# Kernel optimization log

Measured on AMD Instinct MI355X. Metric: run time of the kernel, lower is better.

## Reference

```python
import jax, jax.numpy as jnp
import numpy as np

LOGIT_SCALE_MAX = float(np.log(1.0 / 0.01))  # log(100)
EPS = 1e-12  # F.normalize eps


def setup_inputs() -> dict:
    key = jax.random.key(0)
    ks = jax.random.split(key, 4)
    L, N, C, H = 1024, 8, 1024, 16
    x = jax.random.normal(ks[0], (L, N, C), dtype=jnp.float32)
    w_in = jax.random.normal(ks[1], (3 * C, C), dtype=jnp.float32) * 0.02
    b_in = jnp.zeros((3 * C,), dtype=jnp.float32)
    logit_scale = jnp.full((H, 1, 1), float(np.log(10.0)), dtype=jnp.float32)
    head_scale = jnp.ones((H, 1, 1), dtype=jnp.float32)
    w_out = jax.random.normal(ks[2], (C, C), dtype=jnp.float32) * 0.02
    b_out = jnp.zeros((C,), dtype=jnp.float32)
    return {"x": x, "w_in": w_in, "b_in": b_in, "logit_scale": logit_scale,
            "head_scale": head_scale, "w_out": w_out, "b_out": b_out}


def _l2norm(t):
    # matches F.normalize(t, dim=-1): t / max(||t||, eps)
    n = jnp.sqrt(jnp.sum(t * t, axis=-1, keepdims=True))
    return t / jnp.maximum(n, EPS)


def reference(x, w_in, b_in, logit_scale, head_scale, w_out, b_out):
    L, N, C = x.shape
    H = logit_scale.shape[0]
    D = C // H
    qkv = x @ w_in.T + b_in                      # (L, N, 3C)
    q, k, v = jnp.split(qkv, 3, axis=-1)         # each (L, N, C)

    def to_heads(t):                             # (L, N, C) -> (N*H, L, D)
        return t.reshape(L, N * H, D).transpose(1, 0, 2)

    q, k, v = to_heads(q), to_heads(k), to_heads(v)
    # cosine-similarity logits with clamped learned per-head scale
    attn = jnp.einsum('bld,bmd->blm', _l2norm(q), _l2norm(k))  # (N*H, L, L)
    ls = jnp.exp(jnp.minimum(logit_scale, LOGIT_SCALE_MAX))    # (H,1,1)
    attn = (attn.reshape(N, H, L, L) * ls).reshape(N * H, L, L)
    attn = jax.nn.softmax(attn, axis=-1)
    out = jnp.einsum('blm,bmd->bld', attn, v)    # (N*H, L, D)
    # per-head scaling (intended math of the head_scale branch)
    out = (out.reshape(N, H, L, D) * head_scale).reshape(N * H, L, D)
    out = out.transpose(1, 0, 2).reshape(L, N, C)
    out = out @ w_out.T + b_out
    return out, attn
```

## Files before the change

kernel.cpp:

```cpp
#include <hip/hip_runtime.h>
#include <hip/hip_fp16.h>
#include <cstdint>

typedef _Float16 f16;
typedef _Float16 f16x8 __attribute__((ext_vector_type(8)));
typedef float f32x4 __attribute__((ext_vector_type(4)));

#define MFMA16(a, b, c) __builtin_amdgcn_mfma_f32_16x16x32_f16(a, b, c, 0, 0, 0)

constexpr int Lq = 1024, Nb = 8, Cc = 1024, Hh = 16, Dd = 64;
constexpr int Mrows = Lq * Nb;
constexpr float LOG100 = 4.6051701859880913680f;
constexpr float LOG2E = 1.4426950408889634f;

typedef const __attribute__((address_space(1))) unsigned int* gu32p;
typedef __attribute__((address_space(3))) unsigned int* lu32p;
__device__ __forceinline__ void gl_lds16(const void* g, void* l) {
  __builtin_amdgcn_global_load_lds((gu32p)g, (lu32p)l, 16, 0, 0);
}

__global__ __launch_bounds__(256) void k_cvt(const float* __restrict__ in,
                                             f16* __restrict__ out, int n8) {
  int i = blockIdx.x * blockDim.x + threadIdx.x;
  if (i >= n8) return;
  const float4* p = (const float4*)in + (size_t)i * 2;
  float4 a = p[0], b = p[1];
  f16x8 o = {(f16)a.x, (f16)a.y, (f16)a.z, (f16)a.w,
             (f16)b.x, (f16)b.y, (f16)b.z, (f16)b.w};
  *((f16x8*)out + i) = o;
}

template <typename OutT>
__global__ __launch_bounds__(256) void k_gemm(const f16* __restrict__ A,
                                              const f16* __restrict__ B,
                                              const float* __restrict__ bias,
                                              OutT* __restrict__ Co,
                                              int Np, int Kd) {
  __shared__ f16 Ash[128 * 64];
  __shared__ f16 Bsh[128 * 64];
  const int tid = threadIdx.x, lane = tid & 63, wid = tid >> 6;
  const int m0 = blockIdx.y * 128, n0 = blockIdx.x * 128;
  const int wy = wid >> 1, wx = wid & 1;
  const int rq = lane & 15, kq = lane >> 4;
  f32x4 acc[4][4] = {};
  const int nkt = Kd >> 6;
  for (int kt = 0; kt < nkt; ++kt) {
    __syncthreads();
    for (int iss = 0; iss < 4; ++iss) {
      int cbase = (iss * 4 + wid) * 64;
      int c = cbase + lane;
      int row = ((c >> 7) << 4) + (c & 15);
      int col = kt * 64 + ((c >> 6) & 1) * 32 + ((c >> 4) & 3) * 8;
      gl_lds16(A + (size_t)(m0 + row) * Kd + col, (char*)Ash + cbase * 16);
      gl_lds16(B + (size_t)(n0 + row) * Kd + col, (char*)Bsh + cbase * 16);
    }
    __syncthreads();
    for (int ks = 0; ks < 2; ++ks) {
      f16x8 af[4], bf[4];
      for (int t = 0; t < 4; ++t)
        af[t] = *(const f16x8*)((const char*)Ash + ((((wy * 4 + t) * 2 + ks) * 64 + lane) * 16));
      for (int u = 0; u < 4; ++u)
        bf[u] = *(const f16x8*)((const char*)Bsh + ((((wx * 4 + u) * 2 + ks) * 64 + lane) * 16));
      for (int t = 0; t < 4; ++t)
        for (int u = 0; u < 4; ++u)
          acc[t][u] = MFMA16(af[t], bf[u], acc[t][u]);
    }
  }
  for (int t = 0; t < 4; ++t) {
    int row = m0 + wy * 64 + t * 16 + 4 * kq;
    for (int u = 0; u < 4; ++u) {
      int col = n0 + wx * 64 + u * 16 + rq;
      float bv = bias[col];
      for (int rr = 0; rr < 4; ++rr) {
        float v = acc[t][u][rr] + bv;
        Co[(size_t)(row + rr) * Np + col] = (OutT)v;
      }
    }
  }
}

__global__ __launch_bounds__(256) void k_norm(const f16* __restrict__ qkv,
                                              f16* __restrict__ qhat,
                                              f16* __restrict__ khat,
                                              f16* __restrict__ vTt) {
  __shared__ f16 vt[64][72];
  const int blk = blockIdx.x;
  const int b = blk >> 4, lc = blk & 15;
  const int h = b & 15, n = b >> 4;
  const int tid = threadIdx.x;
  const int g4 = tid >> 2, sub = tid & 3;
  const int lrow = lc * 64 + g4;
  const size_t srow = ((size_t)lrow * Nb + n) * 3072;
  for (int qk = 0; qk < 2; ++qk) {
    const f16* p = qkv + srow + qk * 1024 + h * 64 + sub * 16;
    f16x8 a = *(const f16x8*)p;
    f16x8 c2 = *(const f16x8*)(p + 8);
    float ss = 0.f;
    for (int e = 0; e < 8; ++e) { float x = (float)a[e]; ss += x * x; }
    for (int e = 0; e < 8; ++e) { float x = (float)c2[e]; ss += x * x; }
    ss += __shfl_xor(ss, 1);
    ss += __shfl_xor(ss, 2);
    float sc = 1.f / fmaxf(sqrtf(ss), 1e-12f);
    f16x8 oa, ob;
    for (int e = 0; e < 8; ++e) oa[e] = (f16)((float)a[e] * sc);
    for (int e = 0; e < 8; ++e) ob[e] = (f16)((float)c2[e] * sc);
    f16* dst = (qk ? khat : qhat) + ((size_t)b * Lq + lrow) * Dd + sub * 16;
    *(f16x8*)dst = oa;
    *(f16x8*)(dst + 8) = ob;
  }
  {
    const f16* p = qkv + srow + 2048 + h * 64 + sub * 16;
    f16x8 a = *(const f16x8*)p;
    f16x8 c2 = *(const f16x8*)(p + 8);
    for (int e = 0; e < 8; ++e) vt[g4][sub * 16 + e] = a[e];
    for (int e = 0; e < 8; ++e) vt[g4][sub * 16 + 8 + e] = c2[e];
  }
  __syncthreads();
  {
    const int d = g4;
    f16x8 oa, ob;
    for (int e = 0; e < 8; ++e) oa[e] = vt[sub * 16 + e][d];
    for (int e = 0; e < 8; ++e) ob[e] = vt[sub * 16 + 8 + e][d];
    f16* dst = vTt + ((size_t)b * Dd + d) * Lq + lc * 64 + sub * 16;
    *(f16x8*)dst = oa;
    *(f16x8*)(dst + 8) = ob;
  }
}

__global__ __launch_bounds__(256) void k_attn(const f16* __restrict__ qhat,
                                              const f16* __restrict__ khat,
                                              const f16* __restrict__ vTt,
                                              const float* __restrict__ lsc,
                                              const float* __restrict__ hsc,
                                              float* __restrict__ attn,
                                              f16* __restrict__ Ows) {
  __shared__ float plds[4][16 * 68];
  const int blk = blockIdx.x;
  const int b = blk >> 4, qc = blk & 15;
  const int h = b & 15, n = b >> 4;
  const int tid = threadIdx.x, lane = tid & 63, w = tid >> 6;
  const int rq = lane & 15, kq = lane >> 4;
  const int ib = qc * 64 + w * 16;
  const float ls = __expf(fminf(lsc[h], LOG100));
  const float hs = hsc[h];
  const float c1 = ls * LOG2E, c0 = -c1;
  const f16* qb = qhat + ((size_t)b * Lq + ib) * Dd;
  f16x8 qf0 = *(const f16x8*)(qb + (size_t)rq * Dd + kq * 8);
  f16x8 qf1 = *(const f16x8*)(qb + (size_t)rq * Dd + 32 + kq * 8);
  const f16* kb = khat + (size_t)b * Lq * Dd;
  float lsum[4] = {0.f, 0.f, 0.f, 0.f};
  for (int kt = 0; kt < 16; ++kt) {
    const int j0 = kt * 64;
    f32x4 s[4];
    for (int u = 0; u < 4; ++u) {
      const f16* kp = kb + (size_t)(j0 + u * 16 + rq) * Dd + kq * 8;
      f16x8 k0 = *(const f16x8*)kp;
      f16x8 k1 = *(const f16x8*)(kp + 32);
      f32x4 a = {0.f, 0.f, 0.f, 0.f};
      a = MFMA16(qf0, k0, a);
      a = MFMA16(qf1, k1, a);
      s[u] = a;
    }
    for (int rr = 0; rr < 4; ++rr) {
      float e0 = exp2f(fmaf(s[0][rr], c1, c0));
      float e1 = exp2f(fmaf(s[1][rr], c1, c0));
      float e2 = exp2f(fmaf(s[2][rr], c1, c0));
      float e3 = exp2f(fmaf(s[3][rr], c1, c0));
      lsum[rr] += (e0 + e1) + (e2 + e3);
    }
  }
  float invl[4];
  for (int rr = 0; rr < 4; ++rr) {
    float l = lsum[rr];
    l += __shfl_xor(l, 1);
    l += __shfl_xor(l, 2);
    l += __shfl_xor(l, 4);
    l += __shfl_xor(l, 8);
    invl[rr] = 1.f / l;
  }
  float* pw = plds[w];
  f32x4 Oa[4] = {};
  const f16* vb = vTt + (size_t)b * Dd * Lq;
  float* ab = attn + (size_t)b * Lq * Lq;
  const int srow = lane >> 2, sc4 = lane & 3;
  for (int kt = 0; kt < 16; ++kt) {
    const int j0 = kt * 64;
    f32x4 s[4];
    for (int u = 0; u < 4; ++u) {
      const f16* kp = kb + (size_t)(j0 + u * 16 + rq) * Dd + kq * 8;
      f16x8 k0 = *(const f16x8*)kp;
      f16x8 k1 = *(const f16x8*)(kp + 32);
      f32x4 a = {0.f, 0.f, 0.f, 0.f};
      a = MFMA16(qf0, k0, a);
      a = MFMA16(qf1, k1, a);
      s[u] = a;
    }
    for (int u = 0; u < 4; ++u)
      for (int rr = 0; rr < 4; ++rr) {
        float p = exp2f(fmaf(s[u][rr], c1, c0)) * invl[rr];
        pw[(4 * kq + rr) * 68 + u * 16 + rq] = p;
      }
    {
      const float* lp = pw + srow * 68;
      float* gp = ab + (size_t)(ib + srow) * Lq + j0;
      for (int st = 0; st < 4; ++st) {
        int f4 = st * 4 + sc4;
        f32x4 v = *(const f32x4*)(lp + f4 * 4);
        *(f32x4*)(gp + f4 * 4) = v;
      }
    }
    f16x8 pa[2];
    for (int ks = 0; ks < 2; ++ks) {
      const float* sp = pw + rq * 68 + ks * 32 + kq * 8;
      f16x8 t;
      for (int e = 0; e < 8; ++e) t[e] = (f16)sp[e];
      pa[ks] = t;
    }
    for (int t = 0; t < 4; ++t) {
      const f16* vp = vb + (size_t)(t * 16 + rq) * Lq + j0 + kq * 8;
      f16x8 v0 = *(const f16x8*)vp;
      f16x8 v1 = *(const f16x8*)(vp + 32);
      Oa[t] = MFMA16(pa[0], v0, Oa[t]);
      Oa[t] = MFMA16(pa[1], v1, Oa[t]);
    }
  }
  for (int t = 0; t < 4; ++t) {
    for (int rr = 0; rr < 4; ++rr) {
      int iseq = ib + 4 * kq + rr;
      int d = t * 16 + rq;
      Ows[((size_t)iseq * Nb + n) * Cc + h * Dd + d] = (f16)(Oa[t][rr] * hs);
    }
  }
}

extern "C" void kernel_launch(void* const* d_in, const int* in_sizes, int n_in,
                              void* d_out, int out_size, void* d_ws, size_t ws_size,
                              hipStream_t stream) {
  const float* x     = (const float*)d_in[0];
  const float* w_in  = (const float*)d_in[1];
  const float* b_in  = (const float*)d_in[2];
  const float* lsc   = (const float*)d_in[3];
  const float* hsc   = (const float*)d_in[4];
  const float* w_out = (const float*)d_in[5];
  const float* b_out = (const float*)d_in[6];
  float* out  = (float*)d_out;
  float* attn = out + (size_t)Mrows * Cc;

  char* ws = (char*)d_ws;
  f16* xh   = (f16*)(ws + 0);
  f16* wh   = (f16*)(ws + 16777216);
  f16* wo   = (f16*)(ws + 23068672);
  f16* qkv  = (f16*)(ws + 25165824);
  f16* qhat = (f16*)(ws + 75497472);
  f16* khat = (f16*)(ws + 92274688);
  f16* vTt  = (f16*)(ws + 109051904);
  f16* Ows  = (f16*)(ws + 125829120);
  if (ws_size < 142606336ull) return;

  k_cvt<<<(Mrows * Cc / 8 + 255) / 256, 256, 0, stream>>>(x, xh, Mrows * Cc / 8);
  k_cvt<<<(3072 * 1024 / 8 + 255) / 256, 256, 0, stream>>>(w_in, wh, 3072 * 1024 / 8);
  k_cvt<<<(1024 * 1024 / 8 + 255) / 256, 256, 0, stream>>>(w_out, wo, 1024 * 1024 / 8);
  k_gemm<f16><<<dim3(24, 64), 256, 0, stream>>>(xh, wh, b_in, qkv, 3072, 1024);
  k_norm<<<2048, 256, 0, stream>>>(qkv, qhat, khat, vTt);
  k_attn<<<2048, 256, 0, stream>>>(qhat, khat, vTt, lsc, hsc, attn, Ows);
  k_gemm<float><<<dim3(8, 64), 256, 0, stream>>>(Ows, wo, b_out, out, 1024, 1024);
}
```

Before: 1.068 ms.

## Stage K/V tiles in LDS, fuse PV into first pass, write attn directly

Restructures the attention kernel so the first pass computes unnormalized exp scores, accumulates the row sum and the PV product at once. Normalization by the row sum is applied to the output at the end, which is valid because the logits are cosine similarities with a bounded scale, so no running max is needed. K and V tiles are staged in shared memory with global-to-LDS loads shared by the four waves. The MFMA operands are swapped so each lane owns one query row, which lets the second pass write the normalized fp32 attn values straight to global memory as float4 without an LDS round trip. The aim is to cut redundant global K/V loads and the per-tile LDS shuffle, at the cost of extra block-wide barriers and fp16 rounding of unnormalized P.

```diff
diff --git a/kernel.cpp b/kernel.cpp
--- a/kernel.cpp
+++ b/kernel.cpp
@@ -3,6 +3,7 @@
 #include <cstdint>
 
 typedef _Float16 f16;
+typedef _Float16 f16x4 __attribute__((ext_vector_type(4)));
 typedef _Float16 f16x8 __attribute__((ext_vector_type(8)));
 typedef float f32x4 __attribute__((ext_vector_type(4)));
 
@@ -134,7 +135,9 @@
                                               const float* __restrict__ hsc,
                                               float* __restrict__ attn,
                                               f16* __restrict__ Ows) {
-  __shared__ float plds[4][16 * 68];
+  __shared__ f16 Kst[4096];
+  __shared__ f16 Vst[4096];
+  __shared__ f16 Pst[4][1024];
   const int blk = blockIdx.x;
   const int b = blk >> 4, qc = blk & 15;
   const int h = b & 15, n = b >> 4;
@@ -148,87 +151,95 @@
   f16x8 qf0 = *(const f16x8*)(qb + (size_t)rq * Dd + kq * 8);
   f16x8 qf1 = *(const f16x8*)(qb + (size_t)rq * Dd + 32 + kq * 8);
   const f16* kb = khat + (size_t)b * Lq * Dd;
-  float lsum[4] = {0.f, 0.f, 0.f, 0.f};
+  const f16* vb = vTt + (size_t)b * Dd * Lq;
+  f16* Pw = Pst[w];
+
+  float lsum = 0.f;
+  f32x4 Oa[4] = {};
   for (int kt = 0; kt < 16; ++kt) {
     const int j0 = kt * 64;
+    __syncthreads();
+    for (int iss = 0; iss < 2; ++iss) {
+      int cbase = (iss * 4 + w) * 64;
+      int c = cbase + lane;
+      int rq_ = c & 15, kq_ = (c >> 4) & 3, h_ = (c >> 6) & 1, u_ = c >> 7;
+      gl_lds16(kb + (size_t)(j0 + u_ * 16 + rq_) * Dd + h_ * 32 + kq_ * 8,
+               (char*)Kst + cbase * 16);
+      gl_lds16(vb + (size_t)(u_ * 16 + rq_) * Lq + j0 + h_ * 32 + kq_ * 8,
+               (char*)Vst + cbase * 16);
+    }
+    __syncthreads();
     f32x4 s[4];
     for (int u = 0; u < 4; ++u) {
-      const f16* kp = kb + (size_t)(j0 + u * 16 + rq) * Dd + kq * 8;
-      f16x8 k0 = *(const f16x8*)kp;
-      f16x8 k1 = *(const f16x8*)(kp + 32);
+      f16x8 k0 = *(const f16x8*)(Kst + (u * 128 + lane) * 8);
+      f16x8 k1 = *(const f16x8*)(Kst + (u * 128 + 64 + lane) * 8);
       f32x4 a = {0.f, 0.f, 0.f, 0.f};
-      a = MFMA16(qf0, k0, a);
-      a = MFMA16(qf1, k1, a);
+      a = MFMA16(k0, qf0, a);
+      a = MFMA16(k1, qf1, a);
       s[u] = a;
     }
-    for (int rr = 0; rr < 4; ++rr) {
-      float e0 = exp2f(fmaf(s[0][rr], c1, c0));
-      float e1 = exp2f(fmaf(s[1][rr], c1, c0));
-      float e2 = exp2f(fmaf(s[2][rr], c1, c0));
-      float e3 = exp2f(fmaf(s[3][rr], c1, c0));
-      lsum[rr] += (e0 + e1) + (e2 + e3);
-    }
-  }
-  float invl[4];
-  for (int rr = 0; rr < 4; ++rr) {
-    float l = lsum[rr];
-    l += __shfl_xor(l, 1);
-    l += __shfl_xor(l, 2);
-    l += __shfl_xor(l, 4);
-    l += __shfl_xor(l, 8);
-    invl[rr] = 1.f / l;
-  }
-  float* pw = plds[w];
-  f32x4 Oa[4] = {};
-  const f16* vb = vTt + (size_t)b * Dd * Lq;
-  float* ab = attn + (size_t)b * Lq * Lq;
-  const int srow = lane >> 2, sc4 = lane & 3;
+    for (int u = 0; u < 4; ++u) {
+      f16x4 t4;
+      for (int rr = 0; rr < 4; ++rr) {
+        float e = exp2f(fmaf(s[u][rr], c1, c0));
+        lsum += e;
+        t4[rr] = (f16)e;
+      }
+      int cw = (u >> 1) * 64 + ((2 * u + (kq >> 1)) & 3) * 16 + rq;
+      *(f16x4*)(Pw + cw * 8 + (kq & 1) * 4) = t4;
+    }
+    f16x8 pa0 = *(const f16x8*)(Pw + (kq * 16 + rq) * 8);
+    f16x8 pa1 = *(const f16x8*)(Pw + (64 + kq * 16 + rq) * 8);
+    for (int t = 0; t < 4; ++t) {
+      f16x8 v0 = *(const f16x8*)(Vst + (t * 128 + lane) * 8);
+      f16x8 v1 = *(const f16x8*)(Vst + (t * 128 + 64 + lane) * 8);
+      Oa[t] = MFMA16(pa0, v0, Oa[t]);
+      Oa[t] = MFMA16(pa1, v1, Oa[t]);
+    }
+  }
+  lsum += __shfl_xor(lsum, 16);
+  lsum += __shfl_xor(lsum, 32);
+  const float invl = 1.f / lsum;
+
+  float* ab = attn + (size_t)b * Lq * Lq + (size_t)(ib + rq) * Lq;
   for (int kt = 0; kt < 16; ++kt) {
     const int j0 = kt * 64;
+    __syncthreads();
+    {
+      int cbase = w * 64 + ((lane >> 5) ? 1024 : 0);
+    }
+    for (int iss = 0; iss < 2; ++iss) {
+      int cbase = (iss * 4 + w) * 64;
+      int c = cbase + lane;
+      int rq_ = c & 15, kq_ = (c >> 4) & 3, h_ = (c >> 6) & 1, u_ = c >> 7;
+      gl_lds16(kb + (size_t)(j0 + u_ * 16 + rq_) * Dd + h_ * 32 + kq_ * 8,
+               (char*)Kst + cbase * 16);
+    }
+    __syncthreads();
     f32x4 s[4];
     for (int u = 0; u < 4; ++u) {
-      const f16* kp = kb + (size_t)(j0 + u * 16 + rq) * Dd + kq * 8;
-      f16x8 k0 = *(const f16x8*)kp;
-      f16x8 k1 = *(const f16x8*)(kp + 32);
+      f16x8 k0 = *(const f16x8*)(Kst + (u * 128 + lane) * 8);
+      f16x8 k1 = *(const f16x8*)(Kst + (u * 128 + 64 + lane) * 8);
       f32x4 a = {0.f, 0.f, 0.f, 0.f};
-      a = MFMA16(qf0, k0, a);
-      a = MFMA16(qf1, k1, a);
+      a = MFMA16(k0, qf0, a);
+      a = MFMA16(k1, qf1, a);
       s[u] = a;
     }
-    for (int u = 0; u < 4; ++u)
-      for (int rr = 0; rr < 4; ++rr) {
-        float p = exp2f(fmaf(s[u][rr], c1, c0)) * invl[rr];
-        pw[(4 * kq + rr) * 68 + u * 16 + rq] = p;
-      }
-    {
-      const float* lp = pw + srow * 68;
-      float* gp = ab + (size_t)(ib + srow) * Lq + j0;
-      for (int st = 0; st < 4; ++st) {
-        int f4 = st * 4 + sc4;
-        f32x4 v = *(const f32x4*)(lp + f4 * 4);
-        *(f32x4*)(gp + f4 * 4) = v;
-      }
-    }
-    f16x8 pa[2];
-    for (int ks = 0; ks < 2; ++ks) {
-      const float* sp = pw + rq * 68 + ks * 32 + kq * 8;
-      f16x8 t;
-      for (int e = 0; e < 8; ++e) t[e] = (f16)sp[e];
-      pa[ks] = t;
-    }
-    for (int t = 0; t < 4; ++t) {
-      const f16* vp = vb + (size_t)(t * 16 + rq) * Lq + j0 + kq * 8;
-      f16x8 v0 = *(const f16x8*)vp;
-      f16x8 v1 = *(const f16x8*)(vp + 32);
-      Oa[t] = MFMA16(pa[0], v0, Oa[t]);
-      Oa[t] = MFMA16(pa[1], v1, Oa[t]);
-    }
-  }
+    for (int u = 0; u < 4; ++u) {
+      f32x4 p;
+      for (int rr = 0; rr < 4; ++rr)
+        p[rr] = exp2f(fmaf(s[u][rr], c1, c0)) * invl;
+      *(f32x4*)(ab + j0 + u * 16 + 4 * kq) = p;
+    }
+  }
+
+  float invlO[4];
+  for (int rr = 0; rr < 4; ++rr) invlO[rr] = __shfl(invl, 4 * kq + rr);
   for (int t = 0; t < 4; ++t) {
     for (int rr = 0; rr < 4; ++rr) {
       int iseq = ib + 4 * kq + rr;
       int d = t * 16 + rq;
-      Ows[((size_t)iseq * Nb + n) * Cc + h * Dd + d] = (f16)(Oa[t][rr] * hs);
+      Ows[((size_t)iseq * Nb + n) * Cc + h * Dd + d] = (f16)(Oa[t][rr] * invlO[rr] * hs);
     }
   }
 }
```

Measured after the change: 864.5 us. 1.24x faster.
